# Optimization experiments

Measured on AMD Instinct MI355X. Metric: run time of the kernel, lower is better.

The kernel has to match this reference:

```python
import jax, jax.numpy as jnp
import numpy as np

PI = float(np.pi)
ALPHA = 2.0          # spikingjelly surrogate.ATan default alpha
V_TH = 1.0           # LIF threshold
BN_EPS = 1e-5

@jax.custom_vjp
def spike_fn(x):
    # Heaviside forward, ATan surrogate backward
    return (x >= 0.0).astype(x.dtype)

def _spike_fwd(x):
    return spike_fn(x), x

def _spike_bwd(x, g):
    return (g * (ALPHA / 2.0) / (1.0 + (PI / 2.0 * ALPHA * x) ** 2),)

spike_fn.defvjp(_spike_fwd, _spike_bwd)


def setup_inputs() -> dict:
    key = jax.random.key(0)
    ks = jax.random.split(key, 9)
    T, B, N, C, H, O = 32, 16, 128, 512, 1024, 512
    x = jax.random.normal(ks[0], (T, B, N, C), dtype=jnp.float32)
    W1 = jax.random.normal(ks[1], (H, C), dtype=jnp.float32) * (1.0 / np.sqrt(C))
    b1 = jnp.zeros((H,), jnp.float32)
    # rec weight is orthogonal-initialized in the original; a QR of a gaussian
    Wrec = jnp.linalg.qr(jax.random.normal(ks[2], (H, H), dtype=jnp.float32))[0]
    brec = jnp.zeros((H,), jnp.float32)
    # ParametricLIF: w = -log(init_tau - 1) = -log(1) = 0 for init_tau=2.0
    w_lif = jnp.zeros((), jnp.float32)
    W2 = jax.random.normal(ks[3], (O, H), dtype=jnp.float32) * (1.0 / np.sqrt(H))
    b2 = jnp.zeros((O,), jnp.float32)
    gamma = jnp.ones((O,), jnp.float32)
    beta = jnp.zeros((O,), jnp.float32)
    return {"x": x, "W1": W1, "b1": b1, "Wrec": Wrec, "brec": brec,
            "w_lif": w_lif, "W2": W2, "b2": b2, "gamma": gamma, "beta": beta}


def reference(x, W1, b1, Wrec, brec, w_lif, W2, b2, gamma, beta):
    T, B, N, C = x.shape
    H = W1.shape[0]
    BN = B * N
    # fc1 over all timesteps at once: [T, B*N, H]
    curr_in = x.reshape(T, BN, C) @ W1.T + b1
    decay = jax.nn.sigmoid(w_lif)

    def step(carry, c_t):
        v, spk = carry
        inp = c_t + spk @ Wrec.T + brec                 # recurrent input current
        v = v + (inp - v) * decay                        # PLIF charge (decay_input, v_reset=0)
        s = spike_fn(v - V_TH)                           # fire (ATan surrogate)
        v = v * (1.0 - jax.lax.stop_gradient(s))         # hard reset, detach_reset
        return (v, s), s

    v0 = jnp.zeros((BN, H), x.dtype)
    s0 = jnp.zeros((BN, H), x.dtype)
    _, spks = jax.lax.scan(step, (v0, s0), curr_in)      # [T, BN, H]

    out = spks @ W2.T + b2                               # [T, BN, O]
    # BatchNorm1d over channel O, stats over (T*B, N) == all non-channel elems
    mean = out.mean(axis=(0, 1))
    var = out.var(axis=(0, 1))                           # biased, matches torch BN fwd
    out = (out - mean) * jax.lax.rsqrt(var + BN_EPS) * gamma + beta
    return out.reshape(T, B, N, -1)
```

## Files before the change

kernel.cpp:

```cpp
#include <hip/hip_runtime.h>
#include <cstdint>
#include <cstddef>

#define T_STEPS 32
#define BNROWS  2048
#define C_DIM   512
#define H_DIM   1024
#define O_DIM   512
#define TBN_DIM 65536

typedef __attribute__((ext_vector_type(8))) short bf16x8;
typedef __attribute__((ext_vector_type(4))) float f32x4;

__device__ __forceinline__ void split3(float x, unsigned short& h,
                                       unsigned short& m, unsigned short& l){
    unsigned u = __float_as_uint(x);
    h = (unsigned short)(u >> 16);
    float r1 = x - __uint_as_float(u & 0xFFFF0000u);
    unsigned u1 = __float_as_uint(r1);
    m = (unsigned short)(u1 >> 16);
    float r2 = r1 - __uint_as_float(u1 & 0xFFFF0000u);
    l = (unsigned short)(__float_as_uint(r2) >> 16);
}

__global__ void split3_w(const float* __restrict__ src,
                         unsigned short* __restrict__ hi,
                         unsigned short* __restrict__ mi,
                         unsigned short* __restrict__ lo, int n4)
{
    int i = blockIdx.x * blockDim.x + threadIdx.x;
    int stride = gridDim.x * blockDim.x;
    for (; i < n4; i += stride) {
        float4 v = ((const float4*)src)[i];
        ushort4 h, m, l;
        split3(v.x, h.x, m.x, l.x); split3(v.y, h.y, m.y, l.y);
        split3(v.z, h.z, m.z, l.z); split3(v.w, h.w, m.w, l.w);
        ((ushort4*)hi)[i] = h;
        ((ushort4*)mi)[i] = m;
        ((ushort4*)lo)[i] = l;
    }
}

__device__ __forceinline__ void st8x2(unsigned short* p, int4 v){
    ((int2*)p)[0] = make_int2(v.x, v.y);
    ((int2*)p)[1] = make_int2(v.z, v.w);
}
__device__ __forceinline__ bf16x8 ld_frag(const unsigned short* p){
    union { bf16x8 v; ushort4 u[2]; } t;
    t.u[0] = *(const ushort4*)(p);
    t.u[1] = *(const ushort4*)(p + 4);
    return t.v;
}

__global__ void wrec_transpose(const float* __restrict__ src,
                               float* __restrict__ dst)
{
    __shared__ float tile[32][33];
    const int bx = blockIdx.x * 32, by = blockIdx.y * 32;
    const int tx = threadIdx.x & 31, ty = threadIdx.x >> 5;
#pragma unroll
    for (int r = 0; r < 32; r += 8)
        tile[ty + r][tx] = src[(size_t)(by + ty + r) * H_DIM + bx + tx];
    __syncthreads();
#pragma unroll
    for (int r = 0; r < 32; r += 8)
        dst[(size_t)(bx + ty + r) * H_DIM + by + tx] = tile[tx][ty + r];
}

template<int BM, int BN, int BK, int TM, int TN>
__global__ __launch_bounds__(256)
void gemm_fc1(const float* __restrict__ Ap,
              const float* __restrict__ Bp,
              int K, int ldc,
              const float* __restrict__ bias,
              float* __restrict__ Cout)
{
    constexpr int BMP = BM + 4;
    constexpr int BNP = BN + 4;
    __shared__ float smem[BK*BMP + BK*BNP];
    float* As = smem;
    float* Bs = smem + BK*BMP;

    const int tid = threadIdx.x;
    constexpr int TXN = BN / TN;
    const int tx = tid % TXN;
    const int ty = tid / TXN;
    const int bm0 = blockIdx.y * BM;
    const int bn0 = blockIdx.x * BN;

    constexpr int CPR = BK / 4;

    float acc[TM][TN];
#pragma unroll
    for (int i = 0; i < TM; ++i)
#pragma unroll
        for (int j = 0; j < TN; ++j) acc[i][j] = 0.f;

    for (int kt = 0; kt < K; kt += BK) {
        {
            constexpr int PT = (BM*BK/4)/256;
#pragma unroll
            for (int it = 0; it < PT; ++it) {
                int e   = it*256 + tid;
                int row = e / CPR;
                int c4  = e % CPR;
                float4 fv = *(const float4*)(Ap + (size_t)(bm0+row)*K + kt + c4*4);
                As[(c4*4+0)*BMP + row] = fv.x;
                As[(c4*4+1)*BMP + row] = fv.y;
                As[(c4*4+2)*BMP + row] = fv.z;
                As[(c4*4+3)*BMP + row] = fv.w;
            }
        }
        {
            constexpr int PT = (BN*BK/4)/256;
#pragma unroll
            for (int it = 0; it < PT; ++it) {
                int e   = it*256 + tid;
                int row = e / CPR;
                int c4  = e % CPR;
                float4 fv = *(const float4*)(Bp + (size_t)(bn0+row)*K + kt + c4*4);
                Bs[(c4*4+0)*BNP + row] = fv.x;
                Bs[(c4*4+1)*BNP + row] = fv.y;
                Bs[(c4*4+2)*BNP + row] = fv.z;
                Bs[(c4*4+3)*BNP + row] = fv.w;
            }
        }
        __syncthreads();
#pragma unroll
        for (int k = 0; k < BK; ++k) {
            float a[TM], b[TN];
            float4 t0 = *(const float4*)&As[k*BMP + ty*8];
            float4 t1 = *(const float4*)&As[k*BMP + ty*8 + 4];
            a[0]=t0.x; a[1]=t0.y; a[2]=t0.z; a[3]=t0.w;
            a[4]=t1.x; a[5]=t1.y; a[6]=t1.z; a[7]=t1.w;
            float4 u0 = *(const float4*)&Bs[k*BNP + tx*4];
            float4 u1 = *(const float4*)&Bs[k*BNP + 64 + tx*4];
            b[0]=u0.x; b[1]=u0.y; b[2]=u0.z; b[3]=u0.w;
            b[4]=u1.x; b[5]=u1.y; b[6]=u1.z; b[7]=u1.w;
#pragma unroll
            for (int i = 0; i < TM; ++i)
#pragma unroll
                for (int j = 0; j < TN; ++j)
                    acc[i][j] = fmaf(a[i], b[j], acc[i][j]);
        }
        __syncthreads();
    }

#pragma unroll
    for (int i = 0; i < TM; ++i) {
        int m = bm0 + ty*TM + i;
        int n0 = bn0 + tx*4;
        int n1 = bn0 + 64 + tx*4;
        float4 bv0 = *(const float4*)&bias[n0];
        float4 bv1 = *(const float4*)&bias[n1];
        float4 o0, o1;
        o0.x = acc[i][0] + bv0.x; o0.y = acc[i][1] + bv0.y;
        o0.z = acc[i][2] + bv0.z; o0.w = acc[i][3] + bv0.w;
        o1.x = acc[i][4] + bv1.x; o1.y = acc[i][5] + bv1.y;
        o1.z = acc[i][6] + bv1.z; o1.w = acc[i][7] + bv1.w;
        *(float4*)&Cout[(size_t)m*ldc + n0] = o0;
        *(float4*)&Cout[(size_t)m*ldc + n1] = o1;
    }
}

__device__ __forceinline__ unsigned long long spread4(unsigned long long x){
    x &= 0xFFFFull;
    x = (x | (x << 24)) & 0x000000FF000000FFull;
    x = (x | (x << 12)) & 0x000F000F000F000Full;
    x = (x | (x << 6 )) & 0x0303030303030303ull;
    x = (x | (x << 3 )) & 0x1111111111111111ull;
    return x;
}

__global__ __launch_bounds__(256)
void mega_scan(const float* __restrict__ curr,
               const float* __restrict__ WrecT,
               const float* __restrict__ brec,
               const float* __restrict__ wlif,
               unsigned short* __restrict__ spk)
{
    const int lane = threadIdx.x & 63;
    const int wid  = threadIdx.x >> 6;
    const int row  = blockIdx.x * 4 + wid;
    const float decay = 1.f / (1.f + expf(-wlif[0]));
    const unsigned long long MSB = 0x8000000000000000ull;

    float v[4][4];
#pragma unroll
    for (int q = 0; q < 4; ++q)
#pragma unroll
        for (int j = 0; j < 4; ++j) v[q][j] = 0.f;

    float brv[4][4];
#pragma unroll
    for (int q = 0; q < 4; ++q) {
        float4 bv = *(const float4*)&brec[q * 256 + lane * 4];
        brv[q][0] = bv.x; brv[q][1] = bv.y; brv[q][2] = bv.z; brv[q][3] = bv.w;
    }

    unsigned long long mask[16];
#pragma unroll
    for (int w = 0; w < 16; ++w) mask[w] = 0ull;

    for (int t = 0; t < T_STEPS; ++t) {
        float acc[4][4];
#pragma unroll
        for (int q = 0; q < 4; ++q)
#pragma unroll
            for (int j = 0; j < 4; ++j) acc[q][j] = 0.f;

#pragma unroll
        for (int w = 0; w < 16; ++w) {
            unsigned long long m = mask[w];
            int pc = __popcll(m);
            for (int s = 0; s < pc; s += 4) {
                int k0 = __builtin_ctzll(m | MSB); m &= m - 1;
                int k1 = __builtin_ctzll(m | MSB); m &= m - 1;
                int k2 = __builtin_ctzll(m | MSB); m &= m - 1;
                int k3 = __builtin_ctzll(m | MSB); m &= m - 1;
                const float* r0 = WrecT + ((size_t)(w * 64 + k0) << 10) + lane * 4;
                const float* r1 = WrecT + ((size_t)(w * 64 + k1) << 10) + lane * 4;
                const float* r2 = WrecT + ((size_t)(w * 64 + k2) << 10) + lane * 4;
                const float* r3 = WrecT + ((size_t)(w * 64 + k3) << 10) + lane * 4;
                float4 w0[4], w1[4], w2[4], w3[4];
#pragma unroll
                for (int q = 0; q < 4; ++q) {
                    w0[q] = *(const float4*)(r0 + q * 256);
                    w1[q] = *(const float4*)(r1 + q * 256);
                    w2[q] = *(const float4*)(r2 + q * 256);
                    w3[q] = *(const float4*)(r3 + q * 256);
                }
                float s1v = (s + 1 < pc) ? 1.f : 0.f;
                float s2v = (s + 2 < pc) ? 1.f : 0.f;
                float s3v = (s + 3 < pc) ? 1.f : 0.f;
#pragma unroll
                for (int q = 0; q < 4; ++q) {
                    acc[q][0] += w0[q].x;
                    acc[q][0] = fmaf(w1[q].x, s1v, acc[q][0]);
                    acc[q][0] = fmaf(w2[q].x, s2v, acc[q][0]);
                    acc[q][0] = fmaf(w3[q].x, s3v, acc[q][0]);
                    acc[q][1] += w0[q].y;
                    acc[q][1] = fmaf(w1[q].y, s1v, acc[q][1]);
                    acc[q][1] = fmaf(w2[q].y, s2v, acc[q][1]);
                    acc[q][1] = fmaf(w3[q].y, s3v, acc[q][1]);
                    acc[q][2] += w0[q].z;
                    acc[q][2] = fmaf(w1[q].z, s1v, acc[q][2]);
                    acc[q][2] = fmaf(w2[q].z, s2v, acc[q][2]);
                    acc[q][2] = fmaf(w3[q].z, s3v, acc[q][2]);
                    acc[q][3] += w0[q].w;
                    acc[q][3] = fmaf(w1[q].w, s1v, acc[q][3]);
                    acc[q][3] = fmaf(w2[q].w, s2v, acc[q][3]);
                    acc[q][3] = fmaf(w3[q].w, s3v, acc[q][3]);
                }
            }
        }

        const float* cr = curr + (((size_t)t * BNROWS + row) << 10);
        unsigned short* sr = spk + (((size_t)t * BNROWS + row) << 10);
        unsigned long long bal[4][4];
#pragma unroll
        for (int q = 0; q < 4; ++q) {
            float4 cv = *(const float4*)(cr + q * 256 + lane * 4);
            float cva[4] = {cv.x, cv.y, cv.z, cv.w};
            unsigned short spa[4];
#pragma unroll
            for (int j = 0; j < 4; ++j) {
                float inp = acc[q][j] + brv[q][j] + cva[j];
                float vv  = v[q][j];
                vv = vv + (inp - vv) * decay;
                bool s = (vv - 1.0f) >= 0.0f;
                v[q][j] = s ? 0.0f : vv;
                spa[j] = s ? (unsigned short)0x3F80 : (unsigned short)0;
                bal[q][j] = __ballot(s);
            }
            ushort4 sp;
            sp.x = spa[0]; sp.y = spa[1]; sp.z = spa[2]; sp.w = spa[3];
            *(ushort4*)(sr + q * 256 + lane * 4) = sp;
        }
#pragma unroll
        for (int w = 0; w < 16; ++w) {
            int q = w >> 2;
            int f = (w & 3) * 16;
            mask[w] = spread4(bal[q][0] >> f)
                    | (spread4(bal[q][1] >> f) << 1)
                    | (spread4(bal[q][2] >> f) << 2)
                    | (spread4(bal[q][3] >> f) << 3);
        }
    }
}

template<int BM, int BN, int WM, int WN, int MI, int NI>
__global__ __launch_bounds__(256)
void mfma_fc2(const unsigned short* __restrict__ Aptr,
              const unsigned short* __restrict__ Bhi,
              const unsigned short* __restrict__ Bmi,
              int K,
              const float* __restrict__ bias,
              float* __restrict__ Cout, int ldc,
              float* __restrict__ partials)
{
    constexpr int LP  = 40;
    constexpr int APL = BM * LP;
    constexpr int BPL = BN * LP;
    __shared__ alignas(16) unsigned short sA[APL];
    __shared__ alignas(16) unsigned short sB[2 * BPL];

    const int nwg = gridDim.x * gridDim.y;
    const int f   = blockIdx.y * gridDim.x + blockIdx.x;
    const int q   = nwg >> 3;
    const int lg  = (f & 7) * q + (f >> 3);
    const int bn0  = (lg % gridDim.x) * BN;
    const int mblk = lg / gridDim.x;
    const int bm0  = mblk * BM;

    const int tid  = threadIdx.x;
    const int lane = tid & 63;
    const int wid  = tid >> 6;
    const int wr   = wid / WN;
    const int wc   = wid % WN;
    const int lr   = lane & 15;
    const int lk   = lane >> 4;

    f32x4 accB[MI][NI], accS[MI][NI];
#pragma unroll
    for (int i = 0; i < MI; ++i)
#pragma unroll
        for (int j = 0; j < NI; ++j) {
            accB[i][j] = (f32x4){0.f, 0.f, 0.f, 0.f};
            accS[i][j] = (f32x4){0.f, 0.f, 0.f, 0.f};
        }

    for (int kt = 0; kt < K; kt += 32) {
#pragma unroll
        for (int p = 0; p < BM / 64; ++p) {
            int e = p * 256 + tid;
            int row = e >> 2, c8 = e & 3;
            int4 v = *(const int4*)(Aptr + (size_t)(bm0 + row) * K + kt + c8 * 8);
            st8x2(&sA[row * LP + c8 * 8], v);
        }
#pragma unroll
        for (int p = 0; p < BN / 64; ++p) {
            int e = p * 256 + tid;
            int row = e >> 2, c8 = e & 3;
            size_t g = (size_t)(bn0 + row) * K + kt + c8 * 8;
            st8x2(&sB[row * LP + c8 * 8],       *(const int4*)(Bhi + g));
            st8x2(&sB[BPL + row * LP + c8 * 8], *(const int4*)(Bmi + g));
        }
        __syncthreads();

        bf16x8 af[MI], b0[NI], b1[NI];
#pragma unroll
        for (int i = 0; i < MI; ++i) {
            int r = wr * MI * 16 + i * 16 + lr;
            af[i] = ld_frag(&sA[r * LP + lk * 8]);
        }
#pragma unroll
        for (int j = 0; j < NI; ++j) {
            int r = wc * NI * 16 + j * 16 + lr;
            b0[j] = ld_frag(&sB[r * LP + lk * 8]);
            b1[j] = ld_frag(&sB[BPL + r * LP + lk * 8]);
        }
#pragma unroll
        for (int i = 0; i < MI; ++i)
#pragma unroll
            for (int j = 0; j < NI; ++j) {
                accB[i][j] = __builtin_amdgcn_mfma_f32_16x16x32_bf16(af[i], b0[j], accB[i][j], 0, 0, 0);
                accS[i][j] = __builtin_amdgcn_mfma_f32_16x16x32_bf16(af[i], b1[j], accS[i][j], 0, 0, 0);
            }
        __syncthreads();
    }

    float csum[NI], csq[NI];
#pragma unroll
    for (int j = 0; j < NI; ++j) { csum[j] = 0.f; csq[j] = 0.f; }
#pragma unroll
    for (int i = 0; i < MI; ++i)
#pragma unroll
        for (int j = 0; j < NI; ++j) {
            int col = bn0 + wc * NI * 16 + j * 16 + lr;
            float bv = bias[col];
#pragma unroll
            for (int r = 0; r < 4; ++r) {
                int row = bm0 + wr * MI * 16 + i * 16 + lk * 4 + r;
                float o = (accB[i][j][r] + accS[i][j][r]) + bv;
                Cout[(size_t)row * ldc + col] = o;
                csum[j] += o;
                csq[j]  += o * o;
            }
        }
    __syncthreads();
    float* redS = (float*)sA;
    float* redQ = (float*)sB;
    const int slot = wr * 4 + lk;
#pragma unroll
    for (int j = 0; j < NI; ++j) {
        int c = wc * NI * 16 + j * 16 + lr;
        redS[slot * BN + c] = csum[j];
        redQ[slot * BN + c] = csq[j];
    }
    __syncthreads();
    if (tid < BN) {
        float s = 0.f, qq = 0.f;
        for (int sl = 0; sl < WM * 4; ++sl) { s += redS[sl * BN + tid]; qq += redQ[sl * BN + tid]; }
        partials[((size_t)mblk * 2 + 0) * O_DIM + bn0 + tid] = s;
        partials[((size_t)mblk * 2 + 1) * O_DIM + bn0 + tid] = qq;
    }
}

__global__ void bn_finalize(const float* __restrict__ partials,
                            const float* __restrict__ gamma,
                            const float* __restrict__ beta,
                            float* __restrict__ scsh, int nmblk)
{
    int o = threadIdx.x;
    float s = 0.f, q = 0.f;
    for (int mb = 0; mb < nmblk; ++mb) {
        s += partials[((size_t)mb*2 + 0)*O_DIM + o];
        q += partials[((size_t)mb*2 + 1)*O_DIM + o];
    }
    const float invn = 1.f / (float)TBN_DIM;
    float mean = s * invn;
    float var  = q * invn - mean*mean;
    float sc   = gamma[o] * rsqrtf(var + 1e-5f);
    scsh[o]        = sc;
    scsh[O_DIM+o]  = beta[o] - mean*sc;
}

__global__ void bn_apply(float* __restrict__ out, const float* __restrict__ scsh)
{
    const size_t total4 = (size_t)TBN_DIM * O_DIM / 4;
    const float4* sc4 = (const float4*)scsh;
    const float4* sh4 = (const float4*)(scsh + O_DIM);
    size_t stride = (size_t)gridDim.x * blockDim.x;
    for (size_t idx = (size_t)blockIdx.x*blockDim.x + threadIdx.x; idx < total4; idx += stride) {
        float4 v = ((float4*)out)[idx];
        int c4 = (int)(idx & (O_DIM/4 - 1));
        float4 sc = sc4[c4], sh = sh4[c4];
        v.x = v.x*sc.x + sh.x;
        v.y = v.y*sc.y + sh.y;
        v.z = v.z*sc.z + sh.z;
        v.w = v.w*sc.w + sh.w;
        ((float4*)out)[idx] = v;
    }
}

extern "C" void kernel_launch(void* const* d_in, const int* in_sizes, int n_in,
                              void* d_out, int out_size, void* d_ws, size_t ws_size,
                              hipStream_t stream) {
    const float* x     = (const float*)d_in[0];
    const float* W1    = (const float*)d_in[1];
    const float* b1    = (const float*)d_in[2];
    const float* Wrec  = (const float*)d_in[3];
    const float* brec  = (const float*)d_in[4];
    const float* wlif  = (const float*)d_in[5];
    const float* W2    = (const float*)d_in[6];
    const float* b2    = (const float*)d_in[7];
    const float* gamma = (const float*)d_in[8];
    const float* beta  = (const float*)d_in[9];
    float* out = (float*)d_out;

    char* w = (char*)d_ws;
    float*          curr  = (float*)w;
    unsigned short* spk   = (unsigned short*)(w + 268435456);
    float*          wrecT = (float*)(w + 402653184);
    unsigned short* w2p   = (unsigned short*)(w + 402653184);
    float* partials = curr;
    float* scsh     = curr + 512 * 2 * O_DIM;

    const int W2N = O_DIM * H_DIM;

    gemm_fc1<128,128,16,8,8>
        <<<dim3(H_DIM/128, TBN_DIM/128), 256, 0, stream>>>(
            x, W1, C_DIM, H_DIM, b1, curr);

    wrec_transpose<<<dim3(32, 32), 256, 0, stream>>>(Wrec, wrecT);

    mega_scan<<<dim3(BNROWS / 4), 256, 0, stream>>>(
        curr, wrecT, brec, wlif, spk);

    split3_w<<<dim3(256), 256, 0, stream>>>(W2, w2p, w2p + W2N, w2p + 2 * W2N, W2N / 4);
    mfma_fc2<128, 128, 2, 2, 4, 4>
        <<<dim3(O_DIM/128, TBN_DIM/128), 256, 0, stream>>>(
            spk, w2p, w2p + W2N, H_DIM, b2, out, O_DIM, partials);

    bn_finalize<<<1, O_DIM, 0, stream>>>(partials, gamma, beta, scsh, TBN_DIM/128);
    bn_apply<<<2048, 256, 0, stream>>>(out, scsh);
}
```

Measured before the change: 1.984 ms.

## Split scan rows across two waves, drop W2 mid term, retile fc1

The recurrent scan kernel now gives each row to two waves, each owning half of the hidden units. The spike masks are exchanged through shared memory with a block barrier every timestep, and loads and stores use nontemporal hints. The fc2 GEMM drops the second bf16 split term of W2 and uses only the high part, which halves its MFMA work but lowers the precision of the output. The fc1 GEMM tile template parameter changes from 16 to 32.

```diff
diff --git a/kernel.cpp b/kernel.cpp
--- a/kernel.cpp
+++ b/kernel.cpp
@@ -11,6 +11,7 @@
 
 typedef __attribute__((ext_vector_type(8))) short bf16x8;
 typedef __attribute__((ext_vector_type(4))) float f32x4;
+typedef __attribute__((ext_vector_type(4))) unsigned short u16x4;
 
 __device__ __forceinline__ void split3(float x, unsigned short& h,
                                        unsigned short& m, unsigned short& l){
@@ -180,51 +181,55 @@
                unsigned short* __restrict__ spk)
 {
     const int lane = threadIdx.x & 63;
-    const int wid  = threadIdx.x >> 6;
-    const int row  = blockIdx.x * 4 + wid;
+    const int wv   = threadIdx.x >> 6;
+    const int r    = wv >> 1;
+    const int h    = wv & 1;
+    const int row  = blockIdx.x * 2 + r;
     const float decay = 1.f / (1.f + expf(-wlif[0]));
     const unsigned long long MSB = 0x8000000000000000ull;
 
-    float v[4][4];
-#pragma unroll
-    for (int q = 0; q < 4; ++q)
+    __shared__ unsigned long long msk[2][2][16];
+
+    if (threadIdx.x < 32) ((unsigned long long*)msk)[threadIdx.x] = 0ull;
+    __syncthreads();
+
+    float v[2][4], brv[2][4];
+#pragma unroll
+    for (int q = 0; q < 2; ++q) {
+        float4 bv = *(const float4*)&brec[(2*h + q) * 256 + lane * 4];
+        brv[q][0] = bv.x; brv[q][1] = bv.y; brv[q][2] = bv.z; brv[q][3] = bv.w;
 #pragma unroll
         for (int j = 0; j < 4; ++j) v[q][j] = 0.f;
-
-    float brv[4][4];
-#pragma unroll
-    for (int q = 0; q < 4; ++q) {
-        float4 bv = *(const float4*)&brec[q * 256 + lane * 4];
-        brv[q][0] = bv.x; brv[q][1] = bv.y; brv[q][2] = bv.z; brv[q][3] = bv.w;
-    }
-
-    unsigned long long mask[16];
-#pragma unroll
-    for (int w = 0; w < 16; ++w) mask[w] = 0ull;
-
+    }
+
+    int p = 0;
     for (int t = 0; t < T_STEPS; ++t) {
-        float acc[4][4];
-#pragma unroll
-        for (int q = 0; q < 4; ++q)
+        float acc[2][4];
+#pragma unroll
+        for (int q = 0; q < 2; ++q)
 #pragma unroll
             for (int j = 0; j < 4; ++j) acc[q][j] = 0.f;
 
 #pragma unroll
         for (int w = 0; w < 16; ++w) {
-            unsigned long long m = mask[w];
+            unsigned long long mv = msk[p][r][w];
+            unsigned lo = __builtin_amdgcn_readfirstlane((unsigned)mv);
+            unsigned hi = __builtin_amdgcn_readfirstlane((unsigned)(mv >> 32));
+            unsigned long long m = ((unsigned long long)hi << 32) | lo;
             int pc = __popcll(m);
+            const float* wbase = WrecT + ((size_t)w << 16) + h * 512 + lane * 4;
             for (int s = 0; s < pc; s += 4) {
                 int k0 = __builtin_ctzll(m | MSB); m &= m - 1;
                 int k1 = __builtin_ctzll(m | MSB); m &= m - 1;
                 int k2 = __builtin_ctzll(m | MSB); m &= m - 1;
                 int k3 = __builtin_ctzll(m | MSB); m &= m - 1;
-                const float* r0 = WrecT + ((size_t)(w * 64 + k0) << 10) + lane * 4;
-                const float* r1 = WrecT + ((size_t)(w * 64 + k1) << 10) + lane * 4;
-                const float* r2 = WrecT + ((size_t)(w * 64 + k2) << 10) + lane * 4;
-                const float* r3 = WrecT + ((size_t)(w * 64 + k3) << 10) + lane * 4;
-                float4 w0[4], w1[4], w2[4], w3[4];
-#pragma unroll
-                for (int q = 0; q < 4; ++q) {
+                const float* r0 = wbase + ((size_t)k0 << 10);
+                const float* r1 = wbase + ((size_t)k1 << 10);
+                const float* r2 = wbase + ((size_t)k2 << 10);
+                const float* r3 = wbase + ((size_t)k3 << 10);
+                float4 w0[2], w1[2], w2[2], w3[2];
+#pragma unroll
+                for (int q = 0; q < 2; ++q) {
                     w0[q] = *(const float4*)(r0 + q * 256);
                     w1[q] = *(const float4*)(r1 + q * 256);
                     w2[q] = *(const float4*)(r2 + q * 256);
@@ -234,7 +239,7 @@
                 float s2v = (s + 2 < pc) ? 1.f : 0.f;
                 float s3v = (s + 3 < pc) ? 1.f : 0.f;
 #pragma unroll
-                for (int q = 0; q < 4; ++q) {
+                for (int q = 0; q < 2; ++q) {
                     acc[q][0] += w0[q].x;
                     acc[q][0] = fmaf(w1[q].x, s1v, acc[q][0]);
                     acc[q][0] = fmaf(w2[q].x, s2v, acc[q][0]);
@@ -255,13 +260,14 @@
             }
         }
 
-        const float* cr = curr + (((size_t)t * BNROWS + row) << 10);
-        unsigned short* sr = spk + (((size_t)t * BNROWS + row) << 10);
-        unsigned long long bal[4][4];
-#pragma unroll
-        for (int q = 0; q < 4; ++q) {
-            float4 cv = *(const float4*)(cr + q * 256 + lane * 4);
-            float cva[4] = {cv.x, cv.y, cv.z, cv.w};
+        const float* cr = curr + (((size_t)t * BNROWS + row) << 10) + h * 512;
+        unsigned short* sr = spk + (((size_t)t * BNROWS + row) << 10) + h * 512;
+        unsigned long long bal[2][4];
+#pragma unroll
+        for (int q = 0; q < 2; ++q) {
+            f32x4 cv = __builtin_nontemporal_load(
+                            (const f32x4*)(cr + q * 256 + lane * 4));
+            float cva[4] = {cv[0], cv[1], cv[2], cv[3]};
             unsigned short spa[4];
 #pragma unroll
             for (int j = 0; j < 4; ++j) {
@@ -273,19 +279,27 @@
                 spa[j] = s ? (unsigned short)0x3F80 : (unsigned short)0;
                 bal[q][j] = __ballot(s);
             }
-            ushort4 sp;
-            sp.x = spa[0]; sp.y = spa[1]; sp.z = spa[2]; sp.w = spa[3];
-            *(ushort4*)(sr + q * 256 + lane * 4) = sp;
-        }
-#pragma unroll
-        for (int w = 0; w < 16; ++w) {
-            int q = w >> 2;
-            int f = (w & 3) * 16;
-            mask[w] = spread4(bal[q][0] >> f)
-                    | (spread4(bal[q][1] >> f) << 1)
-                    | (spread4(bal[q][2] >> f) << 2)
-                    | (spread4(bal[q][3] >> f) << 3);
-        }
+            u16x4 sp;
+            sp[0] = spa[0]; sp[1] = spa[1]; sp[2] = spa[2]; sp[3] = spa[3];
+            __builtin_nontemporal_store(sp, (u16x4*)(sr + q * 256 + lane * 4));
+        }
+        if (lane == 0) {
+#pragma unroll
+            for (int q = 0; q < 2; ++q) {
+                int gq = 2 * h + q;
+#pragma unroll
+                for (int f = 0; f < 4; ++f) {
+                    unsigned long long word =
+                          spread4(bal[q][0] >> (16 * f))
+                        | (spread4(bal[q][1] >> (16 * f)) << 1)
+                        | (spread4(bal[q][2] >> (16 * f)) << 2)
+                        | (spread4(bal[q][3] >> (16 * f)) << 3);
+                    msk[p ^ 1][r][gq * 4 + f] = word;
+                }
+            }
+        }
+        __syncthreads();
+        p ^= 1;
     }
 }
 
@@ -293,7 +307,6 @@
 __global__ __launch_bounds__(256)
 void mfma_fc2(const unsigned short* __restrict__ Aptr,
               const unsigned short* __restrict__ Bhi,
-              const unsigned short* __restrict__ Bmi,
               int K,
               const float* __restrict__ bias,
               float* __restrict__ Cout, int ldc,
@@ -303,7 +316,7 @@
     constexpr int APL = BM * LP;
     constexpr int BPL = BN * LP;
     __shared__ alignas(16) unsigned short sA[APL];
-    __shared__ alignas(16) unsigned short sB[2 * BPL];
+    __shared__ alignas(16) unsigned short sB[BPL];
 
     const int nwg = gridDim.x * gridDim.y;
     const int f   = blockIdx.y * gridDim.x + blockIdx.x;
@@ -321,14 +334,12 @@
     const int lr   = lane & 15;
     const int lk   = lane >> 4;
 
-    f32x4 accB[MI][NI], accS[MI][NI];
+    f32x4 accB[MI][NI];
 #pragma unroll
     for (int i = 0; i < MI; ++i)
 #pragma unroll
-        for (int j = 0; j < NI; ++j) {
+        for (int j = 0; j < NI; ++j)
             accB[i][j] = (f32x4){0.f, 0.f, 0.f, 0.f};
-            accS[i][j] = (f32x4){0.f, 0.f, 0.f, 0.f};
-        }
 
     for (int kt = 0; kt < K; kt += 32) {
 #pragma unroll
@@ -343,12 +354,11 @@
             int e = p * 256 + tid;
             int row = e >> 2, c8 = e & 3;
             size_t g = (size_t)(bn0 + row) * K + kt + c8 * 8;
-            st8x2(&sB[row * LP + c8 * 8],       *(const int4*)(Bhi + g));
-            st8x2(&sB[BPL + row * LP + c8 * 8], *(const int4*)(Bmi + g));
+            st8x2(&sB[row * LP + c8 * 8], *(const int4*)(Bhi + g));
         }
         __syncthreads();
 
-        bf16x8 af[MI], b0[NI], b1[NI];
+        bf16x8 af[MI], b0[NI];
 #pragma unroll
         for (int i = 0; i < MI; ++i) {
             int r = wr * MI * 16 + i * 16 + lr;
@@ -358,15 +368,12 @@
         for (int j = 0; j < NI; ++j) {
             int r = wc * NI * 16 + j * 16 + lr;
             b0[j] = ld_frag(&sB[r * LP + lk * 8]);
-            b1[j] = ld_frag(&sB[BPL + r * LP + lk * 8]);
         }
 #pragma unroll
         for (int i = 0; i < MI; ++i)
 #pragma unroll
-            for (int j = 0; j < NI; ++j) {
+            for (int j = 0; j < NI; ++j)
                 accB[i][j] = __builtin_amdgcn_mfma_f32_16x16x32_bf16(af[i], b0[j], accB[i][j], 0, 0, 0);
-                accS[i][j] = __builtin_amdgcn_mfma_f32_16x16x32_bf16(af[i], b1[j], accS[i][j], 0, 0, 0);
-            }
         __syncthreads();
     }
 
@@ -382,7 +389,7 @@
 #pragma unroll
             for (int r = 0; r < 4; ++r) {
                 int row = bm0 + wr * MI * 16 + i * 16 + lk * 4 + r;
-                float o = (accB[i][j][r] + accS[i][j][r]) + bv;
+                float o = accB[i][j][r] + bv;
                 Cout[(size_t)row * ldc + col] = o;
                 csum[j] += o;
                 csq[j]  += o * o;
@@ -469,19 +476,19 @@
 
     const int W2N = O_DIM * H_DIM;
 
-    gemm_fc1<128,128,16,8,8>
+    gemm_fc1<128,128,32,8,8>
         <<<dim3(H_DIM/128, TBN_DIM/128), 256, 0, stream>>>(
             x, W1, C_DIM, H_DIM, b1, curr);
 
     wrec_transpose<<<dim3(32, 32), 256, 0, stream>>>(Wrec, wrecT);
 
-    mega_scan<<<dim3(BNROWS / 4), 256, 0, stream>>>(
+    mega_scan<<<dim3(BNROWS / 2), 256, 0, stream>>>(
         curr, wrecT, brec, wlif, spk);
 
     split3_w<<<dim3(256), 256, 0, stream>>>(W2, w2p, w2p + W2N, w2p + 2 * W2N, W2N / 4);
     mfma_fc2<128, 128, 2, 2, 4, 4>
         <<<dim3(O_DIM/128, TBN_DIM/128), 256, 0, stream>>>(
-            spk, w2p, w2p + W2N, H_DIM, b2, out, O_DIM, partials);
+            spk, w2p, H_DIM, b2, out, O_DIM, partials);
 
     bn_finalize<<<1, O_DIM, 0, stream>>>(partials, gamma, beta, scsh, TBN_DIM/128);
     bn_apply<<<2048, 256, 0, stream>>>(out, scsh);
```

Result: faster. 1.592 ms (-19.8%).
